# Optimization experiments

Hardware: AMD Instinct MI355X
Metric: run time of the kernel (lower is better)

The kernel has to match this reference:

```python
import jax, jax.numpy as jnp
import numpy as np

EPS = 1e-8  # matches F.cosine_similarity eps


def setup_inputs() -> dict:
    key = jax.random.key(0)
    k1, k2 = jax.random.split(key)
    N, D = 4096, 256
    z1 = jax.random.normal(k1, (N, D), dtype=jnp.float32)
    z2 = jax.random.normal(k2, (N, D), dtype=jnp.float32)
    log_temperature = jnp.asarray(np.log(0.07), dtype=jnp.float32)
    return {"z1": z1, "z2": z2, "log_temperature": log_temperature}


def reference(z1, z2, log_temperature):
    N = z1.shape[0]
    z = jnp.concatenate([z1, z2], axis=0)                      # (2N, D)
    # cosine similarity: normalize once, then a single GEMM
    norm = jnp.maximum(jnp.linalg.norm(z, axis=-1, keepdims=True), EPS)
    zn = z / norm
    sim = zn @ zn.T                                            # (2N, 2N)
    diag = jnp.eye(2 * N, dtype=bool)
    sim = jnp.where(diag, -jnp.inf, sim)
    targets = jnp.concatenate([jnp.arange(N, 2 * N), jnp.arange(0, N)])
    logits = sim / jnp.exp(log_temperature)
    logp = jax.nn.log_softmax(logits, axis=-1)                 # (2N, 2N)
    loss = -jnp.mean(jnp.take_along_axis(logp, targets[:, None], axis=1))
    correct = jnp.sum(jnp.argmax(sim, axis=1) == targets).astype(jnp.float32) / 2.0
    return (loss, correct)
```

## Files before the change

kernel.cpp:

```cpp
#include <hip/hip_runtime.h>
#include <hip/hip_fp16.h>

#define NTOT 8192
#define NHALF 4096
#define DIM 256
#define LOG2E 1.4426950408889634f
#define LN2f 0.6931471805599453f
#define NEG_BIG -1e30f
#define COLSPLIT 8
#define BM 128
#define BN 64
#define CPB (NTOT / COLSPLIT)
#define NTILES (CPB / BN)
#define NBLK ((NTOT / BM) * COLSPLIT)

typedef _Float16 half8 __attribute__((ext_vector_type(8)));
typedef float floatx4 __attribute__((ext_vector_type(4)));

__global__ __launch_bounds__(256) void k_normalize(const float* __restrict__ z1,
                                                   const float* __restrict__ z2,
                                                   __half* __restrict__ zn,
                                                   unsigned int* __restrict__ cnt) {
  if (blockIdx.x == 0 && threadIdx.x == 0) *cnt = 0;
  int row = blockIdx.x * 4 + (threadIdx.x >> 6);
  int lane = threadIdx.x & 63;
  const float* src = (row < NHALF) ? (z1 + (size_t)row * DIM)
                                   : (z2 + (size_t)(row - NHALF) * DIM);
  float4 v = ((const float4*)src)[lane];
  float ss = v.x * v.x + v.y * v.y + v.z * v.z + v.w * v.w;
#pragma unroll
  for (int m = 1; m < 64; m <<= 1) ss += __shfl_xor(ss, m);
  float inv = 1.0f / fmaxf(sqrtf(ss), 1e-8f);
  __half2 h0, h1;
  h0.x = __float2half_rn(v.x * inv);
  h0.y = __float2half_rn(v.y * inv);
  h1.x = __float2half_rn(v.z * inv);
  h1.y = __float2half_rn(v.w * inv);
  __half2* dst = (__half2*)(zn + (size_t)row * DIM + lane * 4);
  dst[0] = h0;
  dst[1] = h1;
}

__global__ __launch_bounds__(256, 2) void k_main(
    const __half* __restrict__ zn, const float* __restrict__ logT,
    float* __restrict__ tS, float* __restrict__ pM, float* __restrict__ pL,
    unsigned int* __restrict__ cnt, float* __restrict__ out) {
  __shared__ uint4 lds[BN * 32];
  __shared__ int lastFlag;

  const int bid = blockIdx.x;
  const int rowTile = bid >> 3;
  const int colq = bid & 7;
  const int rowBase = rowTile * BM;
  const int colBase = colq * CPB;
  const int tid = threadIdx.x;
  const int w = tid >> 6;
  const int lane = tid & 63;
  const int quad = lane >> 4;
  const int cl = lane & 15;

  const float invT = expf(-logT[0]);
  const float kk = invT * LOG2E;

  const int R0 = rowBase + w * 32;
  const int off = (R0 < NHALF) ? NHALF : -NHALF;
  const int T0 = R0 + off;

  half8 a[2][8];
#pragma unroll
  for (int ks = 0; ks < 8; ks++) {
    a[0][ks] = *(const half8*)(zn + (size_t)(R0 + cl) * DIM + ks * 32 + quad * 8);
    a[1][ks] = *(const half8*)(zn + (size_t)(R0 + 16 + cl) * DIM + ks * 32 + quad * 8);
  }

  float Mx[8], L[8];
#pragma unroll
  for (int s = 0; s < 8; s++) { Mx[s] = NEG_BIG; L[s] = 0.f; }

  for (int t = 0; t < NTILES; t++) {
    __syncthreads();
#pragma unroll
    for (int i = 0; i < 8; i++) {
      int idx = tid + i * 256;
      int c = idx >> 5, ch = idx & 31;
      int g = colBase + t * BN + c;
      uint4 v = *(const uint4*)(zn + (size_t)g * DIM + ch * 8);
      lds[c * 32 + (ch ^ (c & 7))] = v;
    }
    __syncthreads();

    floatx4 acc[2][4];
#pragma unroll
    for (int rt = 0; rt < 2; rt++)
#pragma unroll
      for (int nt = 0; nt < 4; nt++) acc[rt][nt] = (floatx4){0.f, 0.f, 0.f, 0.f};

#pragma unroll
    for (int nt = 0; nt < 4; nt++) {
      const int bc = nt * 16 + cl;
#pragma unroll
      for (int ks = 0; ks < 8; ks++) {
        const int ch = ks * 4 + quad;
        half8 b = *(const half8*)&lds[bc * 32 + (ch ^ (bc & 7))];
        acc[0][nt] = __builtin_amdgcn_mfma_f32_16x16x32_f16(a[0][ks], b, acc[0][nt], 0, 0, 0);
        acc[1][nt] = __builtin_amdgcn_mfma_f32_16x16x32_f16(a[1][ks], b, acc[1][nt], 0, 0, 0);
      }
    }

    const int colT = colBase + t * BN;
    const int c0 = colT + cl;
#pragma unroll
    for (int rt = 0; rt < 2; rt++) {
#pragma unroll
      for (int r = 0; r < 4; r++) {
        const int s = rt * 4 + r;
        const int grow = R0 + rt * 16 + quad * 4 + r;
        float v0 = acc[rt][0][r], v1 = acc[rt][1][r];
        float v2 = acc[rt][2][r], v3 = acc[rt][3][r];
        v0 = (c0 == grow) ? NEG_BIG : v0;
        v1 = (c0 + 16 == grow) ? NEG_BIG : v1;
        v2 = (c0 + 32 == grow) ? NEG_BIG : v2;
        v3 = (c0 + 48 == grow) ? NEG_BIG : v3;
        Mx[s] = fmaxf(fmaxf(Mx[s], fmaxf(v0, v1)), fmaxf(v2, v3));
        L[s] += (exp2f(v0 * kk) + exp2f(v1 * kk)) + (exp2f(v2 * kk) + exp2f(v3 * kk));
      }
    }
    if ((unsigned)(T0 - colT) < (unsigned)BN) {
#pragma unroll
      for (int rt = 0; rt < 2; rt++)
#pragma unroll
        for (int r = 0; r < 4; r++) {
          const int grow = R0 + rt * 16 + quad * 4 + r;
          const int tc = grow + off;
          if (c0 == tc) tS[grow] = acc[rt][0][r];
          if (c0 + 16 == tc) tS[grow] = acc[rt][1][r];
          if (c0 + 32 == tc) tS[grow] = acc[rt][2][r];
          if (c0 + 48 == tc) tS[grow] = acc[rt][3][r];
        }
    }
  }

#pragma unroll
  for (int s = 0; s < 8; s++) {
    float m = Mx[s], l = L[s];
#pragma unroll
    for (int sh = 1; sh < 16; sh <<= 1) {
      m = fmaxf(m, __shfl_xor(m, sh));
      l += __shfl_xor(l, sh);
    }
    Mx[s] = m;
    L[s] = l;
  }
  if (cl == 0) {
#pragma unroll
    for (int rt = 0; rt < 2; rt++)
#pragma unroll
      for (int r = 0; r < 4; r++) {
        const int grow = R0 + rt * 16 + quad * 4 + r;
        const int s = rt * 4 + r;
        pM[colq * NTOT + grow] = Mx[s];
        pL[colq * NTOT + grow] = L[s];
      }
  }

  __threadfence();
  __syncthreads();
  if (tid == 0) {
    unsigned prev = __hip_atomic_fetch_add(cnt, 1u, __ATOMIC_ACQ_REL,
                                           __HIP_MEMORY_SCOPE_AGENT);
    lastFlag = (prev == (unsigned)(NBLK - 1)) ? 1 : 0;
  }
  __syncthreads();
  if (!lastFlag) return;

  const float4* pM4 = (const float4*)pM;
  const float4* pL4 = (const float4*)pL;
  const float4* tS4 = (const float4*)tS;
  float lossSum = 0.f, corrSum = 0.f;
  for (int it = 0; it < NTOT / (256 * 4); it++) {
    const int r4 = it * 256 + tid;
    float4 m = make_float4(NEG_BIG, NEG_BIG, NEG_BIG, NEG_BIG);
    float4 Ls = make_float4(0.f, 0.f, 0.f, 0.f);
#pragma unroll
    for (int q = 0; q < COLSPLIT; q++) {
      float4 mq = pM4[q * (NTOT / 4) + r4];
      float4 lq = pL4[q * (NTOT / 4) + r4];
      m.x = fmaxf(m.x, mq.x); m.y = fmaxf(m.y, mq.y);
      m.z = fmaxf(m.z, mq.z); m.w = fmaxf(m.w, mq.w);
      Ls.x += lq.x; Ls.y += lq.y; Ls.z += lq.z; Ls.w += lq.w;
    }
    float4 tp = tS4[r4];
    lossSum += (LN2f * log2f(Ls.x) - tp.x * invT) +
               (LN2f * log2f(Ls.y) - tp.y * invT) +
               (LN2f * log2f(Ls.z) - tp.z * invT) +
               (LN2f * log2f(Ls.w) - tp.w * invT);
    corrSum += ((tp.x >= m.x) ? 1.f : 0.f) + ((tp.y >= m.y) ? 1.f : 0.f) +
               ((tp.z >= m.z) ? 1.f : 0.f) + ((tp.w >= m.w) ? 1.f : 0.f);
  }
  float* sl = (float*)lds;
  float* sc = sl + 256;
  sl[tid] = lossSum;
  sc[tid] = corrSum;
  __syncthreads();
  for (int s2 = 128; s2 > 0; s2 >>= 1) {
    if (tid < s2) { sl[tid] += sl[tid + s2]; sc[tid] += sc[tid + s2]; }
    __syncthreads();
  }
  if (tid == 0) {
    out[0] = sl[0] * (1.0f / (float)NTOT);
    out[1] = sc[0] * 0.5f;
  }
}

extern "C" void kernel_launch(void* const* d_in, const int* in_sizes, int n_in,
                              void* d_out, int out_size, void* d_ws, size_t ws_size,
                              hipStream_t stream) {
  const float* z1 = (const float*)d_in[0];
  const float* z2 = (const float*)d_in[1];
  const float* logT = (const float*)d_in[2];

  char* ws = (char*)d_ws;
  __half* zn = (__half*)ws;
  float* tS = (float*)(ws + (size_t)(4 << 20));
  float* pM = (float*)(ws + (size_t)(4 << 20) + (32 << 10));
  float* pL = pM + COLSPLIT * NTOT;
  unsigned int* cnt = (unsigned int*)(pL + COLSPLIT * NTOT);

  k_normalize<<<NTOT / 4, 256, 0, stream>>>(z1, z2, zn, cnt);
  k_main<<<NBLK, 256, 0, stream>>>(zn, logT, tS, pM, pL, cnt, (float*)d_out);
}
```

Measured before the change: 155.5 us.

## Double-buffer B tiles in LDS with register-staged prefetch of next tile

The main loop now keeps two LDS buffers for the column tile. The next tile's global loads are issued into registers before the current tile's MFMA and softmax work, then written to the other buffer afterwards. This hides global load latency behind compute and cuts the loop to one barrier per tile. In exchange it doubles LDS use (about 64KB per block) and adds 32 staging VGPRs, which may affect occupancy under launch_bounds(256,2).

```diff
diff --git a/kernel.cpp b/kernel.cpp
--- a/kernel.cpp
+++ b/kernel.cpp
@@ -45,7 +45,7 @@
     const __half* __restrict__ zn, const float* __restrict__ logT,
     float* __restrict__ tS, float* __restrict__ pM, float* __restrict__ pL,
     unsigned int* __restrict__ cnt, float* __restrict__ out) {
-  __shared__ uint4 lds[BN * 32];
+  __shared__ uint4 lds[2][BN * 32];
   __shared__ int lastFlag;
 
   const int bid = blockIdx.x;
@@ -73,21 +73,32 @@
     a[1][ks] = *(const half8*)(zn + (size_t)(R0 + 16 + cl) * DIM + ks * 32 + quad * 8);
   }
 
+  const int ch = tid & 31;
+  const int c0r = tid >> 5;
+  const int ldsBase = c0r * 32 + (ch ^ (c0r & 7));
+  const __half* gB = zn + (size_t)(colBase + c0r) * DIM + ch * 8;
+
   float Mx[8], L[8];
 #pragma unroll
   for (int s = 0; s < 8; s++) { Mx[s] = NEG_BIG; L[s] = 0.f; }
 
+  uint4 st[8];
+#pragma unroll
+  for (int i = 0; i < 8; i++)
+    st[i] = *(const uint4*)(gB + (size_t)i * 8 * DIM);
+#pragma unroll
+  for (int i = 0; i < 8; i++)
+    lds[0][ldsBase + i * 256] = st[i];
+  __syncthreads();
+
   for (int t = 0; t < NTILES; t++) {
-    __syncthreads();
-#pragma unroll
-    for (int i = 0; i < 8; i++) {
-      int idx = tid + i * 256;
-      int c = idx >> 5, ch = idx & 31;
-      int g = colBase + t * BN + c;
-      uint4 v = *(const uint4*)(zn + (size_t)g * DIM + ch * 8);
-      lds[c * 32 + (ch ^ (c & 7))] = v;
-    }
-    __syncthreads();
+    const int cur = t & 1;
+
+    if (t + 1 < NTILES) {
+#pragma unroll
+      for (int i = 0; i < 8; i++)
+        st[i] = *(const uint4*)(gB + ((size_t)(t + 1) * BN + (size_t)i * 8) * DIM);
+    }
 
     floatx4 acc[2][4];
 #pragma unroll
@@ -100,8 +111,8 @@
       const int bc = nt * 16 + cl;
 #pragma unroll
       for (int ks = 0; ks < 8; ks++) {
-        const int ch = ks * 4 + quad;
-        half8 b = *(const half8*)&lds[bc * 32 + (ch ^ (bc & 7))];
+        const int kc = ks * 4 + quad;
+        half8 b = *(const half8*)&lds[cur][bc * 32 + (kc ^ (bc & 7))];
         acc[0][nt] = __builtin_amdgcn_mfma_f32_16x16x32_f16(a[0][ks], b, acc[0][nt], 0, 0, 0);
         acc[1][nt] = __builtin_amdgcn_mfma_f32_16x16x32_f16(a[1][ks], b, acc[1][nt], 0, 0, 0);
       }
@@ -138,6 +149,13 @@
           if (c0 + 48 == tc) tS[grow] = acc[rt][3][r];
         }
     }
+
+    if (t + 1 < NTILES) {
+#pragma unroll
+      for (int i = 0; i < 8; i++)
+        lds[cur ^ 1][ldsBase + i * 256] = st[i];
+      __syncthreads();
+    }
   }
 
 #pragma unroll
```

Result: no change. 152.6 us (-1.9%).
